# Performance work log

Measured on AMD Instinct MI355X. Metric: run time of the kernel, lower is better.

The kernel has to match this reference:

```python
import jax, jax.numpy as jnp
import numpy as np

TWOPI = 2.0 * np.pi


def setup_inputs() -> dict:
    key = jax.random.key(0)
    B, N, C = 16, 2048, 256
    x = jax.random.normal(key, (B, N, C), dtype=jnp.float32)
    return {"x": x}


def reference(x) -> jnp.ndarray:
    # Real-cosine DFT along dim 1: out[b,k,c] = sum_n x[b,n,c] * cos(-2*pi*n*k/N)
    # Equivalent to the original broadcast+sum but expressed as a GEMM with the
    # precomputed (N, N) cosine matrix (avoids the B*N*N*C intermediate).
    N = x.shape[1]
    n = jnp.arange(N, dtype=x.dtype)
    term = -TWOPI * n[None, :] * n[:, None] / N  # (k, n)
    cos_mat = jnp.cos(term)
    return jnp.einsum('kn,bnc->bkc', cos_mat, x)
```

## Files before the change

### kernel.cpp

```cpp
#include <hip/hip_runtime.h>
#include <hip/hip_bf16.h>
#include <math.h>

typedef __bf16 bf16_t;
typedef __attribute__((ext_vector_type(8))) __bf16 bf16x8;
typedef __attribute__((ext_vector_type(4))) float f32x4;

#define NN 2048
#define CC 256
#define BB 16
#define COLS 4096

#define KEE 320
#define MEE 256
#define KEO 256
#define MEO 256
#define KO  512
#define MO  512

#define ANG2 (6.283185307179586f / 2048.0f)
#define ANG1 (6.283185307179586f / 1024.0f)
#define ANG0 (6.283185307179586f / 512.0f)

__device__ __forceinline__ void gload_lds16(const void* g, void* l) {
    __builtin_amdgcn_global_load_lds(
        (const __attribute__((address_space(1))) void*)g,
        (__attribute__((address_space(3))) void*)l, 16, 0, 0);
}

#define NBLK_AEE 10
#define NBLK_AEO 8
#define NBLK_AO  32
#define NBLK_A   (NBLK_AEE + NBLK_AEO + NBLK_AO)
#define NBLK_FOLD 128
#define PREP_BLOCKS (NBLK_A + NBLK_FOLD)

union V8 { bf16_t h[8]; uint4 v; };

__global__ __launch_bounds__(1024) void prep_kernel(
    const float* __restrict__ x,
    bf16_t* __restrict__ Aee, bf16_t* __restrict__ Aeo, bf16_t* __restrict__ Ao,
    bf16_t* __restrict__ Yee, bf16_t* __restrict__ Yeo, bf16_t* __restrict__ Yo,
    float* __restrict__ out)
{
    __shared__ bf16_t e_lds[32][522];
    __shared__ bf16_t o_lds[32][522];
    __shared__ float red[32][33];
    const int blk = blockIdx.x;
    const int t = threadIdx.x;

    if (blk < NBLK_AEE) {
        const int u = blk * 1024 + t;
        const int i = u / 40;
        const int p0 = (u - i * 40) * 8;
        const unsigned step = (unsigned)i & 511u;
        unsigned ph = ((unsigned)i * (unsigned)p0) & 511u;
        V8 vals;
#pragma unroll
        for (int q = 0; q < 8; ++q) {
            vals.h[q] = (p0 + q <= 256) ? (bf16_t)cosf((float)ph * ANG0) : (bf16_t)0.0f;
            ph = (ph + step) & 511u;
        }
        *reinterpret_cast<uint4*>(Aee + (size_t)i * KEE + p0) = vals.v;
        return;
    }
    if (blk < NBLK_AEE + NBLK_AEO) {
        const int u = (blk - NBLK_AEE) * 1024 + t;
        const int i = u >> 5;
        const int m0 = (u & 31) * 8;
        const unsigned tw = 2u * (unsigned)i + 1u;
        unsigned ph = ((unsigned)m0 * tw) & 1023u;
        V8 vals;
#pragma unroll
        for (int q = 0; q < 8; ++q) {
            vals.h[q] = (bf16_t)cosf((float)ph * ANG1);
            ph = (ph + tw) & 1023u;
        }
        *reinterpret_cast<uint4*>(Aeo + (size_t)i * KEO + m0) = vals.v;
        return;
    }
    if (blk < NBLK_A) {
        const int u = (blk - NBLK_AEE - NBLK_AEO) * 1024 + t;
        const int j = u >> 6;
        const int m0 = (u & 63) * 8;
        const unsigned tw = 2u * (unsigned)j + 1u;
        unsigned ph = ((unsigned)m0 * tw) & 2047u;
        V8 vals;
#pragma unroll
        for (int q = 0; q < 8; ++q) {
            vals.h[q] = (bf16_t)cosf((float)ph * ANG2);
            ph = (ph + tw) & 2047u;
        }
        *reinterpret_cast<uint4*>(Ao + (size_t)j * KO + m0) = vals.v;
        return;
    }

    const int fb = blk - NBLK_A;
    const int gc0 = fb * 32;
    const int b = gc0 >> 8;
    const int c0 = gc0 & 255;
    const int tx = t & 31;
    const int ty = t >> 5;
    const float* xb = x + (size_t)b * NN * CC + c0;

    for (int m0 = 0; m0 <= 512; m0 += 32) {
        const int m = m0 + ty;
        if (m <= 512) {
            const int r2 = 1024 - m, r3 = 1024 + m, r4 = (2048 - m) & 2047;
            const float x1 = xb[(size_t)m  * CC + tx];
            const float x2 = xb[(size_t)r2 * CC + tx];
            const float x3 = xb[(size_t)r3 * CC + tx];
            const float x4 = xb[(size_t)r4 * CC + tx];
            const float w = (m == 0 || m == 512) ? 0.5f : 1.0f;
            e_lds[tx][m] = (bf16_t)(w * ((x1 + x3) + (x2 + x4)));
            if (m <= 511) {
                const float w0 = (m == 0) ? 0.5f : 1.0f;
                o_lds[tx][m] = (bf16_t)(w0 * ((x1 - x3) - (x2 - x4)));
            }
        }
    }
    __syncthreads();

    {
        float part = 0.f;
        for (int p = ty; p <= 256; p += 32) {
            float ee;
            if (p == 0) ee = (float)e_lds[tx][0] + (float)e_lds[tx][512];
            else if (p < 256) ee = (float)e_lds[tx][p] + (float)e_lds[tx][512 - p];
            else ee = (float)e_lds[tx][256];
            part += ee;
        }
        red[ty][tx] = (ty & 1) ? -part : part;
    }
    __syncthreads();
    if (t < 32) {
        float tot = 0.f;
#pragma unroll
        for (int s = 0; s < 32; ++s) tot += red[s][t];
        out[(size_t)b * NN * CC + (size_t)1024 * CC + c0 + t] = tot;
    }

    for (int idx = t; idx < 32 * 136; idx += 1024) {
        const int col = idx & 31;
        const int ch = idx >> 5;
        V8 vals;
        bf16_t* dst;
        if (ch < 40) {
            const int p0 = ch * 8;
#pragma unroll
            for (int q = 0; q < 8; ++q) {
                const int p = p0 + q;
                float v;
                if (p == 0) v = (float)e_lds[col][0] + (float)e_lds[col][512];
                else if (p < 256) v = (float)e_lds[col][p] + (float)e_lds[col][512 - p];
                else if (p == 256) v = (float)e_lds[col][256];
                else v = 0.f;
                vals.h[q] = (bf16_t)v;
            }
            dst = Yee + (size_t)(gc0 + col) * KEE + p0;
        } else if (ch < 72) {
            const int m0 = (ch - 40) * 8;
#pragma unroll
            for (int q = 0; q < 8; ++q) {
                const int m = m0 + q;
                const float v = (m == 0)
                    ? (float)e_lds[col][0] - (float)e_lds[col][512]
                    : (float)e_lds[col][m] - (float)e_lds[col][512 - m];
                vals.h[q] = (bf16_t)v;
            }
            dst = Yeo + (size_t)(gc0 + col) * KEO + m0;
        } else {
            const int m0 = (ch - 72) * 8;
#pragma unroll
            for (int q = 0; q < 8; ++q) vals.h[q] = o_lds[col][m0 + q];
            dst = Yo + (size_t)(gc0 + col) * KO + m0;
        }
        *reinterpret_cast<uint4*>(dst) = vals.v;
    }
}


__global__ __launch_bounds__(256) void gemm_kernel(
    const bf16_t* __restrict__ Aee, const bf16_t* __restrict__ Aeo,
    const bf16_t* __restrict__ Ao,
    const bf16_t* __restrict__ Yee, const bf16_t* __restrict__ Yeo,
    const bf16_t* __restrict__ Yo, float* __restrict__ out)
{
    __shared__ bf16_t As[128 * 64];
    __shared__ bf16_t Bs[64 * 64];

    const int col0 = blockIdx.x * 64;
    const int yb = blockIdx.y;

    const bf16_t *Ab, *Bb;
    int row0, kdim, half;
    if (yb < 4)      { half = 0; row0 = yb * 64;        kdim = KEE; Ab = Aee + (size_t)row0 * KEE; Bb = Yee + (size_t)col0 * KEE; }
    else if (yb < 8) { half = 1; row0 = (yb - 4) * 64;  kdim = KEO; Ab = Aeo + (size_t)row0 * KEO; Bb = Yeo + (size_t)col0 * KEO; }
    else             { half = 2; row0 = (yb - 8) * 128; kdim = KO;  Ab = Ao  + (size_t)row0 * KO;  Bb = Yo  + (size_t)col0 * KO; }
    const int ksteps = kdim >> 6;

    const int t = threadIdx.x;
    const int lane = t & 63;
    const int wid = t >> 6;
    const int wr = wid >> 1, wc = wid & 1;
    const int srow = t >> 3;
    const int scol = (t & 7) * 8;
    const int lrow = lane & 15;
    const int rgrp = lane >> 4;
    const int cl = lane & 15;

    if (half == 2) {
        f32x4 acc[4][2] = {};
        for (int kt = 0; kt < 8; ++kt) {
            const int k0 = kt * 64;
            __syncthreads();
#pragma unroll
            for (int it = 0; it < 4; ++it) {
                const int r = srow + it * 32;
                gload_lds16(Ab + (size_t)r * KO + k0 + scol, As + r * 64 + scol);
            }
#pragma unroll
            for (int it = 0; it < 2; ++it) {
                const int r = srow + it * 32;
                gload_lds16(Bb + (size_t)r * KO + k0 + scol, Bs + r * 64 + scol);
            }
            __syncthreads();
#pragma unroll
            for (int kk = 0; kk < 64; kk += 32) {
                const int koff = kk + (lane >> 4) * 8;
                bf16x8 af[4], bfr[2];
#pragma unroll
                for (int m = 0; m < 4; ++m)
                    af[m] = *(const bf16x8*)&As[(wr * 64 + m * 16 + lrow) * 64 + koff];
#pragma unroll
                for (int n = 0; n < 2; ++n)
                    bfr[n] = *(const bf16x8*)&Bs[(wc * 32 + n * 16 + lrow) * 64 + koff];
#pragma unroll
                for (int m = 0; m < 4; ++m)
#pragma unroll
                    for (int n = 0; n < 2; ++n)
                        acc[m][n] = __builtin_amdgcn_mfma_f32_16x16x32_bf16(
                            af[m], bfr[n], acc[m][n], 0, 0, 0);
            }
        }
#pragma unroll
        for (int m = 0; m < 4; ++m)
#pragma unroll
            for (int n = 0; n < 2; ++n) {
                const int col = col0 + wc * 32 + n * 16 + cl;
                float* obc = out + (size_t)(col >> 8) * NN * CC + (col & 255);
#pragma unroll
                for (int r = 0; r < 4; ++r) {
                    const int j = row0 + wr * 64 + m * 16 + rgrp * 4 + r;
                    const float v = acc[m][n][r];
                    obc[(size_t)(2 * j + 1) * CC] = v;
                    obc[(size_t)(2047 - 2 * j) * CC] = v;
                }
            }
    } else {
        f32x4 acc[2][2] = {};
        for (int kt = 0; kt < ksteps; ++kt) {
            const int k0 = kt * 64;
            __syncthreads();
#pragma unroll
            for (int it = 0; it < 2; ++it) {
                const int r = srow + it * 32;
                gload_lds16(Ab + (size_t)r * kdim + k0 + scol, As + r * 64 + scol);
                gload_lds16(Bb + (size_t)r * kdim + k0 + scol, Bs + r * 64 + scol);
            }
            __syncthreads();
#pragma unroll
            for (int kk = 0; kk < 64; kk += 32) {
                const int koff = kk + (lane >> 4) * 8;
                bf16x8 af[2], bfr[2];
#pragma unroll
                for (int m = 0; m < 2; ++m)
                    af[m] = *(const bf16x8*)&As[(wr * 32 + m * 16 + lrow) * 64 + koff];
#pragma unroll
                for (int n = 0; n < 2; ++n)
                    bfr[n] = *(const bf16x8*)&Bs[(wc * 32 + n * 16 + lrow) * 64 + koff];
#pragma unroll
                for (int m = 0; m < 2; ++m)
#pragma unroll
                    for (int n = 0; n < 2; ++n)
                        acc[m][n] = __builtin_amdgcn_mfma_f32_16x16x32_bf16(
                            af[m], bfr[n], acc[m][n], 0, 0, 0);
            }
        }
#pragma unroll
        for (int m = 0; m < 2; ++m)
#pragma unroll
            for (int n = 0; n < 2; ++n) {
                const int col = col0 + wc * 32 + n * 16 + cl;
                float* obc = out + (size_t)(col >> 8) * NN * CC + (col & 255);
#pragma unroll
                for (int r = 0; r < 4; ++r) {
                    const int i = row0 + wr * 32 + m * 16 + rgrp * 4 + r;
                    const float v = acc[m][n][r];
                    if (half == 0) {
                        obc[(size_t)(4 * i) * CC] = v;
                        if (i >= 1) obc[(size_t)(2048 - 4 * i) * CC] = v;
                    } else {
                        obc[(size_t)(4 * i + 2) * CC] = v;
                        obc[(size_t)(2046 - 4 * i) * CC] = v;
                    }
                }
            }
    }
}


__global__ void fallback_kernel(const float* __restrict__ x, float* __restrict__ out) {
    __shared__ float tbl[NN];
    const int b = blockIdx.y;
    const int kbase = blockIdx.x * 16;
    const int t = threadIdx.x;
    for (int i = t; i < NN; i += 256)
        tbl[i] = cosf((float)i * ANG2);
    __syncthreads();
    float acc[16];
#pragma unroll
    for (int kk = 0; kk < 16; ++kk) acc[kk] = 0.f;
    const float* xb = x + (size_t)b * NN * CC;
    for (int n = 0; n < NN; ++n) {
        const float xv = xb[(size_t)n * CC + t];
#pragma unroll
        for (int kk = 0; kk < 16; ++kk) {
            const int m = (n * (kbase + kk)) & (NN - 1);
            acc[kk] += tbl[m] * xv;
        }
    }
#pragma unroll
    for (int kk = 0; kk < 16; ++kk)
        out[((size_t)b * NN + kbase + kk) * CC + t] = acc[kk];
}

extern "C" void kernel_launch(void* const* d_in, const int* in_sizes, int n_in,
                              void* d_out, int out_size, void* d_ws, size_t ws_size,
                              hipStream_t stream) {
    const float* x = (const float*)d_in[0];
    float* out = (float*)d_out;

    const size_t Aee_b = (size_t)MEE * KEE * 2;
    const size_t Aeo_b = (size_t)MEO * KEO * 2;
    const size_t Ao_b  = (size_t)MO  * KO  * 2;
    const size_t Yee_b = (size_t)COLS * KEE * 2;
    const size_t Yeo_b = (size_t)COLS * KEO * 2;
    const size_t Yo_b  = (size_t)COLS * KO  * 2;
    const size_t need = Aee_b + Aeo_b + Ao_b + Yee_b + Yeo_b + Yo_b;

    if (ws_size >= need) {
        char* p = (char*)d_ws;
        bf16_t* Aee = (bf16_t*)p;              p += Aee_b;
        bf16_t* Aeo = (bf16_t*)p;              p += Aeo_b;
        bf16_t* Ao  = (bf16_t*)p;              p += Ao_b;
        bf16_t* Yee = (bf16_t*)p;              p += Yee_b;
        bf16_t* Yeo = (bf16_t*)p;              p += Yeo_b;
        bf16_t* Yo  = (bf16_t*)p;
        prep_kernel<<<PREP_BLOCKS, 1024, 0, stream>>>(x, Aee, Aeo, Ao, Yee, Yeo, Yo, out);
        gemm_kernel<<<dim3(COLS / 64, 12), 256, 0, stream>>>(Aee, Aeo, Ao, Yee, Yeo, Yo, out);
    } else {
        fallback_kernel<<<dim3(NN / 16, BB), CC, 0, stream>>>(x, out);
    }
}
```

Before: 31.55 us.

## Restructure fold prep into register-only 256-thread blocks and move DC sum to GEMM

```diff
diff --git a/kernel.cpp b/kernel.cpp
--- a/kernel.cpp
+++ b/kernel.cpp
@@ -14,9 +14,7 @@
 #define KEE 320
 #define MEE 256
 #define KEO 256
-#define MEO 256
 #define KO  512
-#define MO  512
 
 #define ANG2 (6.283185307179586f / 2048.0f)
 #define ANG1 (6.283185307179586f / 1024.0f)
@@ -28,29 +26,25 @@
         (__attribute__((address_space(3))) void*)l, 16, 0, 0);
 }
 
-#define NBLK_AEE 10
-#define NBLK_AEO 8
-#define NBLK_AO  32
+union V8 { bf16_t h[8]; uint4 v; };
+
+#define NBLK_AEE 40
+#define NBLK_AEO 32
+#define NBLK_AO  128
 #define NBLK_A   (NBLK_AEE + NBLK_AEO + NBLK_AO)
-#define NBLK_FOLD 128
-#define PREP_BLOCKS (NBLK_A + NBLK_FOLD)
-
-union V8 { bf16_t h[8]; uint4 v; };
-
-__global__ __launch_bounds__(1024) void prep_kernel(
+#define NBLK_FOLD 512
+#define PREP_BLOCKS (NBLK_A + NBLK_FOLD + 64)
+
+__global__ __launch_bounds__(256) void prep_kernel(
     const float* __restrict__ x,
     bf16_t* __restrict__ Aee, bf16_t* __restrict__ Aeo, bf16_t* __restrict__ Ao,
-    bf16_t* __restrict__ Yee, bf16_t* __restrict__ Yeo, bf16_t* __restrict__ Yo,
-    float* __restrict__ out)
+    bf16_t* __restrict__ Yee, bf16_t* __restrict__ Yeo, bf16_t* __restrict__ Yo)
 {
-    __shared__ bf16_t e_lds[32][522];
-    __shared__ bf16_t o_lds[32][522];
-    __shared__ float red[32][33];
     const int blk = blockIdx.x;
     const int t = threadIdx.x;
 
     if (blk < NBLK_AEE) {
-        const int u = blk * 1024 + t;
+        const int u = blk * 256 + t;
         const int i = u / 40;
         const int p0 = (u - i * 40) * 8;
         const unsigned step = (unsigned)i & 511u;
@@ -65,7 +59,7 @@
         return;
     }
     if (blk < NBLK_AEE + NBLK_AEO) {
-        const int u = (blk - NBLK_AEE) * 1024 + t;
+        const int u = (blk - NBLK_AEE) * 256 + t;
         const int i = u >> 5;
         const int m0 = (u & 31) * 8;
         const unsigned tw = 2u * (unsigned)i + 1u;
@@ -80,102 +74,90 @@
         return;
     }
     if (blk < NBLK_A) {
-        const int u = (blk - NBLK_AEE - NBLK_AEO) * 1024 + t;
+        const int u = (blk - NBLK_AEE - NBLK_AEO) * 256 + t;
         const int j = u >> 6;
-        const int m0 = (u & 63) * 8;
+        const int u0 = (u & 63) * 8;
         const unsigned tw = 2u * (unsigned)j + 1u;
-        unsigned ph = ((unsigned)m0 * tw) & 2047u;
         V8 vals;
 #pragma unroll
         for (int q = 0; q < 8; ++q) {
+            const int uu = u0 + q;
+            const int m = (uu <= 256) ? uu : (768 - uu);
+            const unsigned ph = ((unsigned)m * tw) & 2047u;
             vals.h[q] = (bf16_t)cosf((float)ph * ANG2);
-            ph = (ph + tw) & 2047u;
-        }
-        *reinterpret_cast<uint4*>(Ao + (size_t)j * KO + m0) = vals.v;
-        return;
-    }
-
-    const int fb = blk - NBLK_A;
-    const int gc0 = fb * 32;
-    const int b = gc0 >> 8;
-    const int c0 = gc0 & 255;
-    const int tx = t & 31;
-    const int ty = t >> 5;
-    const float* xb = x + (size_t)b * NN * CC + c0;
-
-    for (int m0 = 0; m0 <= 512; m0 += 32) {
-        const int m = m0 + ty;
-        if (m <= 512) {
-            const int r2 = 1024 - m, r3 = 1024 + m, r4 = (2048 - m) & 2047;
-            const float x1 = xb[(size_t)m  * CC + tx];
-            const float x2 = xb[(size_t)r2 * CC + tx];
-            const float x3 = xb[(size_t)r3 * CC + tx];
-            const float x4 = xb[(size_t)r4 * CC + tx];
-            const float w = (m == 0 || m == 512) ? 0.5f : 1.0f;
-            e_lds[tx][m] = (bf16_t)(w * ((x1 + x3) + (x2 + x4)));
-            if (m <= 511) {
-                const float w0 = (m == 0) ? 0.5f : 1.0f;
-                o_lds[tx][m] = (bf16_t)(w0 * ((x1 - x3) - (x2 - x4)));
-            }
-        }
-    }
-    __syncthreads();
+        }
+        *reinterpret_cast<uint4*>(Ao + (size_t)j * KO + u0) = vals.v;
+        return;
+    }
+
+    if (blk < NBLK_A + NBLK_FOLD) {
+        const int f = blk - NBLK_A;
+        const int pt = f >> 6;
+        const int ct = f & 63;
+        const int gc0 = ct * 64;
+        const int col = t & 63;
+        const int pg = t >> 6;
+        const int p_base = pt * 32 + pg * 8;
+        const float* xcol = x + (size_t)(gc0 >> 8) * NN * CC + (gc0 & 255) + col;
+
+        float eeV[8], eoV[8], olV[8], ohV[8];
+#pragma unroll
+        for (int q = 0; q < 8; ++q) {
+            const int p = p_base + q;
+            const int n2 = 512 - p, n3 = 512 + p, n4 = 1024 - p;
+            const int n5 = 1024 + p, n6 = 1536 - p, n7 = 1536 + p;
+            const int n8 = (2048 - p) & 2047;
+            const float x1 = xcol[(size_t)p  * CC];
+            const float x2 = xcol[(size_t)n2 * CC];
+            const float x3 = xcol[(size_t)n3 * CC];
+            const float x4 = xcol[(size_t)n4 * CC];
+            const float x5 = xcol[(size_t)n5 * CC];
+            const float x6 = xcol[(size_t)n6 * CC];
+            const float x7 = xcol[(size_t)n7 * CC];
+            const float x8 = xcol[(size_t)n8 * CC];
+            const float w = (p == 0) ? 0.5f : 1.0f;
+            const float e_lo = w * ((x1 + x4) + (x5 + x8));
+            const float e_hi = w * ((x2 + x3) + (x6 + x7));
+            olV[q] = w * ((x1 - x5) - (x4 - x8));
+            ohV[q] = (x2 - x6) - (x3 - x7);
+            eeV[q] = e_lo + e_hi;
+            eoV[q] = e_lo - e_hi;
+        }
+        if (pt == 0 && pg == 0) {
+            const float a = xcol[(size_t)256  * CC];
+            const float b2 = xcol[(size_t)768  * CC];
+            const float c = xcol[(size_t)1280 * CC];
+            const float d = xcol[(size_t)1792 * CC];
+            ohV[0] = (a - c) - (b2 - d);
+        }
+        V8 vee, veo, vol, voh;
+#pragma unroll
+        for (int q = 0; q < 8; ++q) {
+            vee.h[q] = (bf16_t)eeV[q]; veo.h[q] = (bf16_t)eoV[q];
+            vol.h[q] = (bf16_t)olV[q]; voh.h[q] = (bf16_t)ohV[q];
+        }
+        const size_t gcol = (size_t)(gc0 + col);
+        *reinterpret_cast<uint4*>(Yee + gcol * KEE + p_base) = vee.v;
+        *reinterpret_cast<uint4*>(Yeo + gcol * KEO + p_base) = veo.v;
+        *reinterpret_cast<uint4*>(Yo  + gcol * KO  + p_base) = vol.v;
+        *reinterpret_cast<uint4*>(Yo  + gcol * KO  + 256 + p_base) = voh.v;
+        return;
+    }
 
     {
-        float part = 0.f;
-        for (int p = ty; p <= 256; p += 32) {
-            float ee;
-            if (p == 0) ee = (float)e_lds[tx][0] + (float)e_lds[tx][512];
-            else if (p < 256) ee = (float)e_lds[tx][p] + (float)e_lds[tx][512 - p];
-            else ee = (float)e_lds[tx][256];
-            part += ee;
-        }
-        red[ty][tx] = (ty & 1) ? -part : part;
-    }
-    __syncthreads();
-    if (t < 32) {
-        float tot = 0.f;
-#pragma unroll
-        for (int s = 0; s < 32; ++s) tot += red[s][t];
-        out[(size_t)b * NN * CC + (size_t)1024 * CC + c0 + t] = tot;
-    }
-
-    for (int idx = t; idx < 32 * 136; idx += 1024) {
-        const int col = idx & 31;
-        const int ch = idx >> 5;
-        V8 vals;
-        bf16_t* dst;
-        if (ch < 40) {
-            const int p0 = ch * 8;
-#pragma unroll
-            for (int q = 0; q < 8; ++q) {
-                const int p = p0 + q;
-                float v;
-                if (p == 0) v = (float)e_lds[col][0] + (float)e_lds[col][512];
-                else if (p < 256) v = (float)e_lds[col][p] + (float)e_lds[col][512 - p];
-                else if (p == 256) v = (float)e_lds[col][256];
-                else v = 0.f;
-                vals.h[q] = (bf16_t)v;
-            }
-            dst = Yee + (size_t)(gc0 + col) * KEE + p0;
-        } else if (ch < 72) {
-            const int m0 = (ch - 40) * 8;
-#pragma unroll
-            for (int q = 0; q < 8; ++q) {
-                const int m = m0 + q;
-                const float v = (m == 0)
-                    ? (float)e_lds[col][0] - (float)e_lds[col][512]
-                    : (float)e_lds[col][m] - (float)e_lds[col][512 - m];
-                vals.h[q] = (bf16_t)v;
-            }
-            dst = Yeo + (size_t)(gc0 + col) * KEO + m0;
-        } else {
-            const int m0 = (ch - 72) * 8;
-#pragma unroll
-            for (int q = 0; q < 8; ++q) vals.h[q] = o_lds[col][m0 + q];
-            dst = Yo + (size_t)(gc0 + col) * KO + m0;
-        }
-        *reinterpret_cast<uint4*>(dst) = vals.v;
+        const int ct = blk - (NBLK_A + NBLK_FOLD);
+        if (t >= 64) return;
+        const int gc0 = ct * 64;
+        const float* xcol = x + (size_t)(gc0 >> 8) * NN * CC + (gc0 & 255) + t;
+        const float ee256 = (xcol[(size_t)256 * CC] + xcol[(size_t)768 * CC]) +
+                            (xcol[(size_t)1280 * CC] + xcol[(size_t)1792 * CC]);
+        bf16_t* base = Yee + (size_t)(gc0 + t) * KEE + 256;
+        V8 z; z.v = make_uint4(0, 0, 0, 0);
+        V8 first = z; first.h[0] = (bf16_t)ee256;
+        *reinterpret_cast<uint4*>(base) = first.v;
+#pragma unroll
+        for (int ch = 1; ch < 8; ++ch)
+            *reinterpret_cast<uint4*>(base + ch * 8) = z.v;
     }
 }
 
@@ -188,9 +170,33 @@
 {
     __shared__ bf16_t As[128 * 64];
     __shared__ bf16_t Bs[64 * 64];
+    __shared__ float red[64][4];
 
     const int col0 = blockIdx.x * 64;
     const int yb = blockIdx.y;
+    const int t = threadIdx.x;
+
+    if (yb == 12) {
+        const int col = t & 63;
+        const int part = t >> 6;
+        const bf16_t* yc = Yee + (size_t)(col0 + col) * KEE + part * 80;
+        float s = 0.f;
+#pragma unroll
+        for (int jc = 0; jc < 10; ++jc) {
+            const bf16x8 v = *reinterpret_cast<const bf16x8*>(yc + jc * 8);
+#pragma unroll
+            for (int q = 0; q < 8; ++q)
+                s += (q & 1) ? -(float)v[q] : (float)v[q];
+        }
+        red[col][part] = s;
+        __syncthreads();
+        if (t < 64) {
+            const float tot = (red[t][0] + red[t][1]) + (red[t][2] + red[t][3]);
+            const int gc = col0 + t;
+            out[(size_t)(gc >> 8) * NN * CC + (size_t)1024 * CC + (gc & 255)] = tot;
+        }
+        return;
+    }
 
     const bf16_t *Ab, *Bb;
     int row0, kdim, half;
@@ -199,7 +205,6 @@
     else             { half = 2; row0 = (yb - 8) * 128; kdim = KO;  Ab = Ao  + (size_t)row0 * KO;  Bb = Yo  + (size_t)col0 * KO; }
     const int ksteps = kdim >> 6;
 
-    const int t = threadIdx.x;
     const int lane = t & 63;
     const int wid = t >> 6;
     const int wr = wid >> 1, wc = wid & 1;
@@ -342,8 +347,8 @@
     float* out = (float*)d_out;
 
     const size_t Aee_b = (size_t)MEE * KEE * 2;
-    const size_t Aeo_b = (size_t)MEO * KEO * 2;
-    const size_t Ao_b  = (size_t)MO  * KO  * 2;
+    const size_t Aeo_b = (size_t)256 * KEO * 2;
+    const size_t Ao_b  = (size_t)512 * KO  * 2;
     const size_t Yee_b = (size_t)COLS * KEE * 2;
     const size_t Yeo_b = (size_t)COLS * KEO * 2;
     const size_t Yo_b  = (size_t)COLS * KO  * 2;
@@ -357,8 +362,8 @@
         bf16_t* Yee = (bf16_t*)p;              p += Yee_b;
         bf16_t* Yeo = (bf16_t*)p;              p += Yeo_b;
         bf16_t* Yo  = (bf16_t*)p;
-        prep_kernel<<<PREP_BLOCKS, 1024, 0, stream>>>(x, Aee, Aeo, Ao, Yee, Yeo, Yo, out);
-        gemm_kernel<<<dim3(COLS / 64, 12), 256, 0, stream>>>(Aee, Aeo, Ao, Yee, Yeo, Yo, out);
+        prep_kernel<<<PREP_BLOCKS, 256, 0, stream>>>(x, Aee, Aeo, Ao, Yee, Yeo, Yo);
+        gemm_kernel<<<dim3(COLS / 64, 13), 256, 0, stream>>>(Aee, Aeo, Ao, Yee, Yeo, Yo, out);
     } else {
         fallback_kernel<<<dim3(NN / 16, BB), CC, 0, stream>>>(x, out);
     }
```

New measurement: 28.19 us. 1.12x faster.
